# Optimization experiments

Measured on AMD Instinct MI355X. Metric: run time of the kernel, lower is better.

## Reference

```python
import jax, jax.numpy as jnp
import numpy as np
import math

C_S = 384; C_Z = 128; C_H = 16; H = 12; PQ = 4; PV = 8; C_SURF = 16
N_RES = 512; N_SURF = 2048; B = 1
INF = 1e5; EPS = 1e-8
SOFTPLUS_INV_1 = 0.541324854612918


def _quat_to_rot(q):
    q = q / jnp.linalg.norm(q, axis=-1, keepdims=True)
    w, x, y, z = q[..., 0], q[..., 1], q[..., 2], q[..., 3]
    R = jnp.stack([
        1 - 2 * (y * y + z * z), 2 * (x * y - w * z), 2 * (x * z + w * y),
        2 * (x * y + w * z), 1 - 2 * (x * x + z * z), 2 * (y * z - w * x),
        2 * (x * z - w * y), 2 * (y * z + w * x), 1 - 2 * (x * x + y * y),
    ], axis=-1)
    return R.reshape(q.shape[:-1] + (3, 3))


def setup_inputs() -> dict:
    key = jax.random.key(0)
    ks = jax.random.split(key, 32)
    hc = H * C_H            # 192
    hpq = H * PQ * 3        # 144
    hpkv = H * (PQ + PV) * 3  # 432
    cz4 = C_Z // 4
    concat = hc + H * PV * 3 + H * PV + H * cz4 + hc  # 1152
    w = lambda k, i, o: jax.random.normal(k, (i, o), jnp.float32) * 0.02
    inp = {
        's': jax.random.normal(ks[0], (B, N_RES, C_S), jnp.float32),
        'z': jax.random.normal(ks[1], (B, N_RES, N_RES, C_Z), jnp.float32),
        'rots': _quat_to_rot(jax.random.normal(ks[2], (B, N_RES, 4), jnp.float32)),
        'trans': jax.random.normal(ks[3], (B, N_RES, 3), jnp.float32) * 10.0,
        'mask': jnp.ones((B, N_RES), jnp.float32),
        'surface_points': jax.random.normal(ks[4], (B, N_SURF, 3), jnp.float32) * 10.0,
        'surface_features': jax.random.normal(ks[5], (B, N_SURF, C_SURF), jnp.float32),
        'surface_mask': jnp.ones((B, N_SURF), jnp.float32),
        'Wq': w(ks[6], C_S, hc), 'bq': jnp.zeros((hc,)),
        'Wkv': w(ks[7], C_S, 2 * hc), 'bkv': jnp.zeros((2 * hc,)),
        'Wqp': w(ks[8], C_S, hpq), 'bqp': jnp.zeros((hpq,)),
        'Wkvp': w(ks[9], C_S, hpkv), 'bkvp': jnp.zeros((hpkv,)),
        'Wse': w(ks[10], C_SURF, C_S), 'bse': jnp.zeros((C_S,)),
        'Wsq': w(ks[11], C_S, hc), 'bsq': jnp.zeros((hc,)),
        'Wsk': w(ks[12], C_S, hc), 'bsk': jnp.zeros((hc,)),
        'Wsv': w(ks[13], C_S, hc), 'bsv': jnp.zeros((hc,)),
        'Wb': w(ks[14], C_Z, H), 'bb': jnp.zeros((H,)),
        'Wdz': w(ks[15], C_Z, cz4), 'bdz': jnp.zeros((cz4,)),
        'head_weights': jnp.full((H,), SOFTPLUS_INV_1, jnp.float32),
        'sb_weights': jnp.full((1,), SOFTPLUS_INV_1, jnp.float32),
        'Wout': w(ks[16], concat, C_S), 'bout': jnp.zeros((C_S,)),
        'Wso': w(ks[17], 2 * C_S, C_SURF), 'bso': jnp.zeros((C_SURF,)),
    }
    return inp


def reference(s, z, rots, trans, mask, surface_points, surface_features, surface_mask,
              Wq, bq, Wkv, bkv, Wqp, bqp, Wkvp, bkvp, Wse, bse, Wsq, bsq, Wsk, bsk,
              Wsv, bsv, Wb, bb, Wdz, bdz, head_weights, sb_weights, Wout, bout, Wso, bso):
    lin = lambda x, W, b: x @ W + b
    b_, n, _ = s.shape
    m = surface_points.shape[-2]

    surface_feat = lin(surface_features, Wse, bse)                    # [B,M,c_s]
    # backbone<->surface squared distances
    disp = trans[:, :, None, :] - surface_points[:, None, :, :]       # [B,N,M,3]
    dist_sq = jnp.sum(disp * disp, -1)                                # [B,N,M]

    q = lin(s, Wq, bq).reshape(b_, n, H, C_H)
    kv = lin(s, Wkv, bkv).reshape(b_, n, H, 2 * C_H)
    k, v = kv[..., :C_H], kv[..., C_H:]

    # query points: split into 3 coord chunks, stack, rigid-apply
    qp = lin(s, Wqp, bqp)
    qp = jnp.stack(jnp.split(qp, 3, axis=-1), axis=-1)                # [B,N,H*PQ,3]
    qp = jnp.einsum('bnij,bnpj->bnpi', rots, qp) + trans[:, :, None]
    qp = qp.reshape(b_, n, H, PQ, 3)

    kvp = lin(s, Wkvp, bkvp)
    kvp = jnp.stack(jnp.split(kvp, 3, axis=-1), axis=-1)              # [B,N,H*(PQ+PV),3]
    kvp = jnp.einsum('bnij,bnpj->bnpi', rots, kvp) + trans[:, :, None]
    kvp = kvp.reshape(b_, n, H, PQ + PV, 3)
    kp, vp = kvp[..., :PQ, :], kvp[..., PQ:, :]

    b_bias = lin(z, Wb, bb)                                           # [B,N,N,H]
    a = jnp.einsum('bihc,bjhc->bhij', q, k) * math.sqrt(1.0 / (3 * C_H))
    a = a + math.sqrt(1.0 / 3) * jnp.transpose(b_bias, (0, 3, 1, 2))

    # point-distance attention term
    pt = jnp.sum((qp[:, :, None] - kp[:, None]) ** 2, axis=-1)        # [B,N,N,H,PQ]
    hw = jax.nn.softplus(head_weights)                                # [H]
    pt = jnp.sum(pt, axis=-1) * hw * math.sqrt(1.0 / (3 * (PQ * 9.0 / 2))) * (-0.5)
    a = a + jnp.transpose(pt, (0, 3, 1, 2))                           # [B,H,N,N]

    sq_mask = INF * (mask[:, :, None] * mask[:, None, :] - 1.0)
    a = jax.nn.softmax(a + sq_mask[:, None], axis=-1)

    o = jnp.einsum('bhij,bjhc->bihc', a, v).reshape(b_, n, H * C_H)
    o_pt = jnp.einsum('bhij,bjhpd->bihpd', a, vp)                     # [B,N,H,PV,3]
    o_pt = jnp.einsum('bnji,bnhpj->bnhpi', rots, o_pt - trans[:, :, None, None])
    o_pt_norm = jnp.sqrt(jnp.sum(o_pt ** 2, -1) + EPS).reshape(b_, n, H * PV)
    o_pt_flat = o_pt.reshape(b_, n, H * PV, 3)

    pair_z = lin(z, Wdz, bdz)                                         # [B,N,N,cz/4]
    o_pair = jnp.einsum('bhij,bijc->bihc', a, pair_z).reshape(b_, n, -1)

    # surface cross-attention branch
    sq = lin(s, Wsq, bsq).reshape(b_, n, H, C_H)
    sk = lin(surface_feat, Wsk, bsk).reshape(b_, m, H, C_H)
    sv = lin(surface_feat, Wsv, bsv).reshape(b_, m, H, C_H)
    logits = jnp.einsum('bnhc,bmhc->bhnm', sq, sk) * math.sqrt(1.0 / C_H)
    sbw = jax.nn.softplus(sb_weights)[0]
    logits = logits - 0.5 * sbw * dist_sq[:, None]
    cross_mask = mask[:, :, None] * surface_mask[:, None, :]          # [B,N,M]
    logits = logits + INF * (cross_mask - 1.0)[:, None]
    a_s = jax.nn.softmax(logits, axis=-1)
    o_surf = jnp.einsum('bhnm,bmhc->bnhc', a_s, sv).reshape(b_, n, H * C_H)

    o_cat = jnp.concatenate([o, o_pt_flat[..., 0], o_pt_flat[..., 1], o_pt_flat[..., 2],
                             o_pt_norm, o_pair, o_surf], axis=-1)
    s_out = lin(o_cat, Wout, bout)                                    # [B,N,c_s]

    # surface update: attend surface points to backbone (softmax over residues)
    a_ts = jax.nn.softmax(jnp.swapaxes(logits, -1, -2), axis=-1).mean(axis=1)  # [B,M,N]
    s_agg = jnp.einsum('bmn,bnc->bmc', a_ts, s)
    surf_out = lin(jnp.concatenate([surface_feat, s_agg], axis=-1), Wso, bso)
    return s_out, surf_out
```

## Files before the change

kernel.cpp:

```cpp
#include <hip/hip_runtime.h>
#include <cstddef>


#define CS 384
#define INFV 100000.0f

__device__ __forceinline__ float softplusf(float x) { return log1pf(__expf(x)); }

__global__ __launch_bounds__(256) void k_pack(
    const float* __restrict__ Wq, const float* __restrict__ Wsq,
    const float* __restrict__ Wkv, const float* __restrict__ Wqp,
    const float* __restrict__ Wkvp, const float* __restrict__ Wsk,
    const float* __restrict__ Wsv, const float* __restrict__ Wout,
    const float* __restrict__ bq, const float* __restrict__ bsq,
    const float* __restrict__ bkv, const float* __restrict__ bqp,
    const float* __restrict__ bkvp, const float* __restrict__ bsk,
    const float* __restrict__ bsv,
    float* __restrict__ wt1, float* __restrict__ wt2, float* __restrict__ wt3,
    float* __restrict__ b1, float* __restrict__ b2)
{
    const int b = blockIdx.x, t = threadIdx.x;
    if (b >= 1092) {
        int idx = (b - 1092) * 256 + t;
        if (idx < 1344) {
            float v;
            if (idx < 192) v = bq[idx];
            else if (idx < 384) v = bsq[idx - 192];
            else if (idx < 768) v = bkv[idx - 384];
            else if (idx < 912) v = bqp[idx - 768];
            else v = bkvp[idx - 912];
            b1[idx] = v;
        } else if (idx < 1728) {
            int i2 = idx - 1344;
            b2[i2] = (i2 < 192) ? bsk[i2] : bsv[i2 - 192];
        }
        return;
    }
    const float* src; float* dst; int C, coff, tile, ldd;
    if (b < 72)       { src = Wq;   C = 192; dst = wt1; coff = 0;   ldd = 384;  tile = b; }
    else if (b < 144) { src = Wsq;  C = 192; dst = wt1; coff = 192; ldd = 384;  tile = b - 72; }
    else if (b < 288) { src = Wkv;  C = 384; dst = wt1; coff = 384; ldd = 384;  tile = b - 144; }
    else if (b < 348) { src = Wqp;  C = 144; dst = wt1; coff = 768; ldd = 384;  tile = b - 288; }
    else if (b < 516) { src = Wkvp; C = 432; dst = wt1; coff = 912; ldd = 384;  tile = b - 348; }
    else if (b < 588) { src = Wsk;  C = 192; dst = wt2; coff = 0;   ldd = 384;  tile = b - 516; }
    else if (b < 660) { src = Wsv;  C = 192; dst = wt2; coff = 192; ldd = 384;  tile = b - 588; }
    else              { src = Wout; C = 384; dst = wt3; coff = 0;   ldd = 1152; tile = b - 660; }
    const int cT = (C + 31) >> 5;
    const int tk = tile / cT, tc = tile % cT;
    __shared__ float l[32][33];
    const int tr = t >> 5, tcc = t & 31;
    #pragma unroll
    for (int rr = 0; rr < 4; ++rr) {
        int kloc = tr * 4 + rr;
        int cg = tc * 32 + tcc;
        l[kloc][tcc] = (cg < C) ? src[(size_t)(tk * 32 + kloc) * C + cg] : 0.f;
    }
    __syncthreads();
    #pragma unroll
    for (int rr = 0; rr < 4; ++rr) {
        int cloc = tr * 4 + rr;
        int cg = tc * 32 + cloc;
        if (cg < C) dst[(size_t)(coff + cg) * ldd + tk * 32 + tcc] = l[tcc][cloc];
    }
}

__global__ __launch_bounds__(256) void k_packz(
    const float* __restrict__ Wb, const float* __restrict__ bb,
    const float* __restrict__ Wdz, const float* __restrict__ bdz,
    float* __restrict__ wz, float* __restrict__ bz)
{
    const float s3 = 0.5773502691896258f;
    int idx = blockIdx.x * 256 + threadIdx.x;
    if (idx < 5632) {
        int c = idx >> 7, kk = idx & 127;
        wz[idx] = (c < 12) ? s3 * Wb[kk * 12 + c] : Wdz[kk * 32 + (c - 12)];
    } else if (idx < 5676) {
        int c = idx - 5632;
        bz[c] = (c < 12) ? s3 * bb[c] : bdz[c - 12];
    }
}

__global__ __launch_bounds__(256) void k_transp(
    const float* __restrict__ A, float* __restrict__ At)
{
    __shared__ float tile[32][33];
    const int r0 = blockIdx.y * 32, c0 = blockIdx.x * 32;
    const int tr = threadIdx.x >> 5, tc = threadIdx.x & 31;
    #pragma unroll
    for (int rr = 0; rr < 4; ++rr)
        tile[tr + rr * 8][tc] = A[(size_t)(r0 + tr + rr * 8) * 384 + c0 + tc];
    __syncthreads();
    #pragma unroll
    for (int rr = 0; rr < 4; ++rr)
        At[(size_t)(c0 + tr + rr * 8) * 512 + r0 + tc] = tile[tc][tr + rr * 8];
}

template<int KTOT, bool HB>
__global__ __launch_bounds__(256) void k_gemm(
    const float* __restrict__ A, const float* __restrict__ Wt,
    const float* __restrict__ bias, float* __restrict__ C, int ldc)
{
    __shared__ float As[64][68];
    __shared__ float Ws[64][68];
    const int t = threadIdx.x;
    const int c0 = blockIdx.x * 64, m0 = blockIdx.y * 64;
    const int sr = t >> 4, sk4 = (t & 15) << 2;
    const int wid = t >> 6, lane = t & 63;
    const int wr = (wid >> 1) * 32, wc = (wid & 1) * 32;
    const int lr = lane >> 3, lc = lane & 7;
    float acc[4][4];
    #pragma unroll
    for (int j = 0; j < 4; ++j) {
        float bv = HB ? bias[c0 + wc + lc + 8 * j] : 0.f;
        #pragma unroll
        for (int i = 0; i < 4; ++i) acc[i][j] = bv;
    }
    for (int kc = 0; kc < KTOT; kc += 64) {
        __syncthreads();
        #pragma unroll
        for (int rep = 0; rep < 4; ++rep) {
            int row = sr + rep * 16;
            *(float4*)&As[row][sk4] = *(const float4*)&A[(size_t)(m0 + row) * KTOT + kc + sk4];
            *(float4*)&Ws[row][sk4] = *(const float4*)&Wt[(size_t)(c0 + row) * KTOT + kc + sk4];
        }
        __syncthreads();
        #pragma unroll 4
        for (int k4 = 0; k4 < 16; ++k4) {
            float4 a[4], w[4];
            #pragma unroll
            for (int i = 0; i < 4; ++i) a[i] = *(float4*)&As[wr + lr + 8 * i][k4 * 4];
            #pragma unroll
            for (int j = 0; j < 4; ++j) w[j] = *(float4*)&Ws[wc + lc + 8 * j][k4 * 4];
            #pragma unroll
            for (int i = 0; i < 4; ++i) {
                #pragma unroll
                for (int j = 0; j < 4; ++j) {
                    acc[i][j] = fmaf(a[i].x, w[j].x, acc[i][j]);
                    acc[i][j] = fmaf(a[i].y, w[j].y, acc[i][j]);
                    acc[i][j] = fmaf(a[i].z, w[j].z, acc[i][j]);
                    acc[i][j] = fmaf(a[i].w, w[j].w, acc[i][j]);
                }
            }
        }
    }
    #pragma unroll
    for (int i = 0; i < 4; ++i) {
        #pragma unroll
        for (int j = 0; j < 4; ++j)
            C[(size_t)(m0 + wr + lr + 8 * i) * ldc + c0 + wc + lc + 8 * j] = acc[i][j];
    }
}

__global__ __launch_bounds__(256) void k_scatter(
    const float* __restrict__ proj, const float* __restrict__ rots,
    const float* __restrict__ trans,
    float* __restrict__ qw, float* __restrict__ kw, float* __restrict__ vw,
    float* __restrict__ sqw, float* __restrict__ qpw, float* __restrict__ kpw,
    float* __restrict__ vpw)
{
    __shared__ float p[4][1344];
    const int n0 = blockIdx.x * 4, t = threadIdx.x;
    for (int idx = t; idx < 1344; idx += 256) {
        #pragma unroll
        for (int r = 0; r < 4; ++r) p[r][idx] = proj[(size_t)(n0 + r) * 1344 + idx];
    }
    __syncthreads();
    for (int idx = t; idx < 3072; idx += 256) {
        int r = idx / 768, c = idx % 768;
        int n = n0 + r;
        float v = p[r][c];
        if (c < 192) qw[(size_t)n * 192 + c] = v;
        else if (c < 384) sqw[(size_t)n * 192 + (c - 192)] = v;
        else {
            int cc = c - 384, h = cc >> 5, sub = cc & 31;
            if (sub < 16) kw[(size_t)n * 192 + h * 16 + sub] = v;
            else          vw[(size_t)n * 192 + h * 16 + (sub - 16)] = v;
        }
    }
    for (int idx = t; idx < 2304; idx += 256) {
        int r = idx / 576, rem = idx % 576;
        int n = n0 + r;
        const float* R = &rots[(size_t)n * 9];
        const float* tr = &trans[(size_t)n * 3];
        if (rem < 144) {
            int pp = rem / 3, d = rem % 3;
            float v = fmaf(R[d*3+0], p[r][768 + pp],
                      fmaf(R[d*3+1], p[r][768 + 48 + pp],
                      fmaf(R[d*3+2], p[r][768 + 96 + pp], tr[d])));
            qpw[(size_t)n * 144 + pp * 3 + d] = v;
        } else {
            int rem2 = rem - 144; int pp = rem2 / 3, d = rem2 % 3;
            float v = fmaf(R[d*3+0], p[r][912 + pp],
                      fmaf(R[d*3+1], p[r][912 + 144 + pp],
                      fmaf(R[d*3+2], p[r][912 + 288 + pp], tr[d])));
            int h = pp / 12, ii = pp % 12;
            if (ii < 4) kpw[(size_t)n * 144 + h * 12 + ii * 3 + d] = v;
            else        vpw[(size_t)n * 288 + h * 24 + (ii - 4) * 3 + d] = v;
        }
    }
}

__global__ __launch_bounds__(256) void k_sfeat(
    const float* __restrict__ sf, const float* __restrict__ Wse,
    const float* __restrict__ bse, float* __restrict__ sfeat)
{
    __shared__ float wl[16 * 384];
    __shared__ float sfl[8][16];
    const int m0 = blockIdx.x * 8, t = threadIdx.x;
    for (int idx = t; idx < 6144; idx += 256) wl[idx] = Wse[idx];
    if (t < 128) sfl[t >> 4][t & 15] = sf[(size_t)(m0 + (t >> 4)) * 16 + (t & 15)];
    __syncthreads();
    #pragma unroll
    for (int u = 0; u < 12; ++u) {
        int idx = t + u * 256;
        int r = idx / 384, c = idx % 384;
        float a = bse[c];
        #pragma unroll
        for (int kk = 0; kk < 16; ++kk) a = fmaf(sfl[r][kk], wl[kk * 384 + c], a);
        sfeat[(size_t)(m0 + r) * 384 + c] = a;
    }
}

__global__ __launch_bounds__(256) void k_zpass(
    const float* __restrict__ z, const float* __restrict__ wz,
    const float* __restrict__ bz, float* __restrict__ bpz)
{
    __shared__ float zt[64][132];
    const int i = blockIdx.x, t = threadIdx.x;
    const int jbase = blockIdx.y * 256;
    const int jl = t & 63;
    const int cgs = __builtin_amdgcn_readfirstlane(t >> 6);
    const float* __restrict__ wp = wz + cgs * 11 * 128;
    float bv[11];
    #pragma unroll
    for (int u = 0; u < 11; ++u) bv[u] = bz[cgs * 11 + u];
    for (int ch = 0; ch < 4; ++ch) {
        const int j0 = jbase + ch * 64;
        __syncthreads();
        for (int idx = t; idx < 2048; idx += 256) {
            int r = idx >> 5, c4 = (idx & 31) << 2;
            *(float4*)&zt[r][c4] = *(const float4*)&z[((size_t)i * 512 + j0 + r) * 128 + c4];
        }
        __syncthreads();
        float acc[11];
        #pragma unroll
        for (int u = 0; u < 11; ++u) acc[u] = bv[u];
        #pragma unroll 2
        for (int k4 = 0; k4 < 128; k4 += 4) {
            float4 zv = *(float4*)&zt[jl][k4];
            #pragma unroll
            for (int u = 0; u < 11; ++u) {
                const float* w = wp + u * 128 + k4;
                acc[u] = fmaf(zv.x, w[0],
                         fmaf(zv.y, w[1],
                         fmaf(zv.z, w[2],
                         fmaf(zv.w, w[3], acc[u]))));
            }
        }
        #pragma unroll
        for (int u = 0; u < 11; ++u)
            bpz[((size_t)i * 44 + cgs * 11 + u) * 512 + j0 + jl] = acc[u];
    }
}

__global__ __launch_bounds__(256) void k_attn_a(
    const float* __restrict__ qw, const float* __restrict__ kw,
    const float* __restrict__ qpw, const float* __restrict__ kpw,
    const float* __restrict__ bpz, const float* __restrict__ mask,
    const float* __restrict__ hwp, float* __restrict__ abuf)
{
    __shared__ float pls[4][520];
    __shared__ float qs[64], qps[48], cpt4[4];
    const int i = blockIdx.x, hg = blockIdx.y;
    const int t = threadIdx.x;
    if (t < 64) qs[t] = qw[(size_t)i * 192 + hg * 64 + t];
    if (t < 48) qps[t] = qpw[(size_t)i * 144 + hg * 48 + t];
    if (t < 4) cpt4[t] = -0.5f * 0.13608276348795434f * softplusf(hwp[hg * 4 + t]);
    const float mask_i = mask[i];
    __syncthreads();
    #pragma unroll 2
    for (int it = 0; it < 8; ++it) {
        int idx = t + it * 256;
        int hh = idx >> 9, j = idx & 511;
        int h = hg * 4 + hh;
        float kj[16], kpj[12];
        { const float4* kr = (const float4*)&kw[(size_t)j * 192 + h * 16];
          *(float4*)&kj[0] = kr[0]; *(float4*)&kj[4] = kr[1];
          *(float4*)&kj[8] = kr[2]; *(float4*)&kj[12] = kr[3]; }
        { const float4* kr = (const float4*)&kpw[(size_t)j * 144 + h * 12];
          *(float4*)&kpj[0] = kr[0]; *(float4*)&kpj[4] = kr[1]; *(float4*)&kpj[8] = kr[2]; }
        float qk = 0.f;
        #pragma unroll
        for (int c = 0; c < 16; ++c) qk = fmaf(qs[hh * 16 + c], kj[c], qk);
        float pts = 0.f;
        #pragma unroll
        for (int p = 0; p < 4; ++p) {
            float dx = qps[hh*12+p*3+0] - kpj[p*3+0];
            float dy = qps[hh*12+p*3+1] - kpj[p*3+1];
            float dz = qps[hh*12+p*3+2] - kpj[p*3+2];
            pts += dx*dx + dy*dy + dz*dz;
        }
        float lg = fmaf(0.14433756729740643f, qk, bpz[((size_t)i * 44 + h) * 512 + j]);
        lg = fmaf(cpt4[hh], pts, lg);
        lg += INFV * (mask_i * mask[j] - 1.0f);
        pls[hh][j] = lg;
    }
    __syncthreads();
    const int w = t >> 6, lane = t & 63;
    float v[8];
    #pragma unroll
    for (int k = 0; k < 8; ++k) v[k] = pls[w][lane + k * 64];
    float mx = v[0];
    #pragma unroll
    for (int k = 1; k < 8; ++k) mx = fmaxf(mx, v[k]);
    #pragma unroll
    for (int off = 32; off; off >>= 1) mx = fmaxf(mx, __shfl_xor(mx, off));
    float sm = 0.f;
    #pragma unroll
    for (int k = 0; k < 8; ++k) { v[k] = __expf(v[k] - mx); sm += v[k]; }
    #pragma unroll
    for (int off = 32; off; off >>= 1) sm += __shfl_xor(sm, off);
    const float inv = 1.0f / sm;
    float* dst = abuf + ((size_t)(hg * 4 + w) * 512 + i) * 512;
    #pragma unroll
    for (int k = 0; k < 8; ++k) dst[lane + k * 64] = v[k] * inv;
}

__global__ __launch_bounds__(256) void k_attn_pair(
    const float* __restrict__ abuf, const float* __restrict__ bpz,
    float* __restrict__ ocat)
{
    __shared__ float al[12][512];
    const int i = blockIdx.x, t = threadIdx.x;
    #pragma unroll
    for (int u = 0; u < 12; ++u) {
        al[u][t] = abuf[(size_t)u * 262144 + (size_t)i * 512 + t];
        al[u][t + 256] = abuf[(size_t)u * 262144 + (size_t)i * 512 + t + 256];
    }
    __syncthreads();
    const int c = t & 31;
    const int h1 = t >> 5;
    const bool dual = (t < 128);
    const float* pz = bpz + ((size_t)i * 44 + 12 + c) * 512;
    const float* a1 = al[h1];
    const float* a2 = al[dual ? h1 + 8 : 0];
    float acc1 = 0.f, acc2 = 0.f;
    for (int j = 0; j < 512; j += 4) {
        float4 p = *(const float4*)&pz[j];
        acc1 = fmaf(a1[j+0], p.x, acc1);
        acc1 = fmaf(a1[j+1], p.y, acc1);
        acc1 = fmaf(a1[j+2], p.z, acc1);
        acc1 = fmaf(a1[j+3], p.w, acc1);
        if (dual) {
            acc2 = fmaf(a2[j+0], p.x, acc2);
            acc2 = fmaf(a2[j+1], p.y, acc2);
            acc2 = fmaf(a2[j+2], p.z, acc2);
            acc2 = fmaf(a2[j+3], p.w, acc2);
        }
    }
    ocat[(size_t)i * 1152 + 576 + h1 * 32 + c] = acc1;
    if (dual) ocat[(size_t)i * 1152 + 576 + (h1 + 8) * 32 + c] = acc2;
}

__global__ __launch_bounds__(256) void k_gemm_ov(
    const float* __restrict__ abuf, const float* __restrict__ vw,
    const float* __restrict__ vpw, float* __restrict__ cbuf)
{
    __shared__ float As[64][68];
    __shared__ float Bs[64][44];
    const int i0 = blockIdx.x * 64, h = blockIdx.y;
    const int t = threadIdx.x;
    const int sr = t >> 4, sk4 = (t & 15) << 2;
    const int r1 = t >> 3;
    const int cb = t & 7;
    float acc[2][5];
    #pragma unroll
    for (int u = 0; u < 5; ++u) { acc[0][u] = 0.f; acc[1][u] = 0.f; }
    for (int kc = 0; kc < 512; kc += 64) {
        __syncthreads();
        #pragma unroll
        for (int rep = 0; rep < 4; ++rep) {
            int row = sr + rep * 16;
            *(float4*)&As[row][sk4] =
                *(const float4*)&abuf[(size_t)h * 262144 + (size_t)(i0 + row) * 512 + kc + sk4];
        }
        #pragma unroll
        for (int u = 0; u < 10; ++u) {
            int idx = t + u * 256;
            int r = idx / 40, cc = idx % 40;
            Bs[r][cc] = (cc < 16) ? vw[(size_t)(kc + r) * 192 + h * 16 + cc]
                                  : vpw[(size_t)(kc + r) * 288 + h * 24 + (cc - 16)];
        }
        __syncthreads();
        #pragma unroll 4
        for (int kk = 0; kk < 64; ++kk) {
            float av1 = As[r1][kk], av2 = As[r1 + 32][kk];
            #pragma unroll
            for (int u = 0; u < 5; ++u) {
                float b = Bs[kk][cb + 8 * u];
                acc[0][u] = fmaf(av1, b, acc[0][u]);
                acc[1][u] = fmaf(av2, b, acc[1][u]);
            }
        }
    }
    #pragma unroll
    for (int u = 0; u < 5; ++u) {
        cbuf[((size_t)h * 512 + i0 + r1) * 40 + cb + 8 * u] = acc[0][u];
        cbuf[((size_t)h * 512 + i0 + r1 + 32) * 40 + cb + 8 * u] = acc[1][u];
    }
}

__global__ __launch_bounds__(256) void k_optfin(
    const float* __restrict__ cbuf, const float* __restrict__ rots,
    const float* __restrict__ trans, float* __restrict__ ocat)
{
    __shared__ float cl[4][12][40];
    const int i0 = blockIdx.x * 4, t = threadIdx.x;
    for (int idx = t; idx < 1920; idx += 256) {
        int ii = idx / 480, rem = idx % 480;
        int h = rem / 40, c = rem % 40;
        cl[ii][h][c] = cbuf[((size_t)h * 512 + i0 + ii) * 40 + c];
    }
    __syncthreads();
    for (int idx = t; idx < 768; idx += 256) {
        int ii = idx / 192, o = idx % 192;
        ocat[(size_t)(i0 + ii) * 1152 + o] = cl[ii][o >> 4][o & 15];
    }
    for (int idx = t; idx < 384; idx += 256) {
        int ii = idx / 96, hp = idx % 96;
        int h = hp >> 3, p = hp & 7;
        int i = i0 + ii;
        const float* R = &rots[(size_t)i * 9];
        float gx = cl[ii][h][16 + p*3 + 0] - trans[(size_t)i*3 + 0];
        float gy = cl[ii][h][16 + p*3 + 1] - trans[(size_t)i*3 + 1];
        float gz = cl[ii][h][16 + p*3 + 2] - trans[(size_t)i*3 + 2];
        float lx = R[0]*gx + R[3]*gy + R[6]*gz;
        float ly = R[1]*gx + R[4]*gy + R[7]*gz;
        float lz = R[2]*gx + R[5]*gy + R[8]*gz;
        float nm = sqrtf(lx*lx + ly*ly + lz*lz + 1e-8f);
        int col = h * 8 + p;
        size_t base = (size_t)i * 1152;
        ocat[base + 192 + col] = lx;
        ocat[base + 288 + col] = ly;
        ocat[base + 384 + col] = lz;
        ocat[base + 480 + col] = nm;
    }
}

__global__ __launch_bounds__(256) void k_tlog(
    const float* __restrict__ sqw, const float* __restrict__ skv,
    const float* __restrict__ trans, const float* __restrict__ mask,
    const float* __restrict__ sp, const float* __restrict__ smask,
    const float* __restrict__ sbwp, float* __restrict__ logits,
    float* __restrict__ stat_m, float* __restrict__ stat_il)
{
    __shared__ float sk_s[32][16];
    __shared__ float sq_s[32][16];
    __shared__ float trans_s[96];
    __shared__ float mask_s[32];
    __shared__ float spm_s[96];
    __shared__ float smask_s[32];
    const int h = blockIdx.y;
    const int m0 = blockIdx.x * 32;
    const int t = threadIdx.x;
    const int tmg = t >> 5, tnl = t & 31;
    const float sbw = softplusf(sbwp[0]);
    for (int idx = t; idx < 512; idx += 256) {
        int row = idx >> 4, c = idx & 15;
        sk_s[row][c] = skv[(size_t)(m0 + row) * 384 + h * 16 + c];
    }
    if (t < 96) spm_s[t] = sp[(size_t)m0 * 3 + t];
    if (t < 32) smask_s[t] = smask[m0 + t];
    __syncthreads();
    float skr[4][16];
    float spx[4], spy[4], spz[4], smk[4];
    #pragma unroll
    for (int mi = 0; mi < 4; ++mi) {
        int row = tmg * 4 + mi;
        #pragma unroll
        for (int c4 = 0; c4 < 16; c4 += 4)
            *(float4*)&skr[mi][c4] = *(float4*)&sk_s[row][c4];
        spx[mi] = spm_s[row*3+0]; spy[mi] = spm_s[row*3+1]; spz[mi] = spm_s[row*3+2];
        smk[mi] = smask_s[row];
    }
    float mxr[4], lr[4];
    #pragma unroll
    for (int mi = 0; mi < 4; ++mi) { mxr[mi] = -1e30f; lr[mi] = 0.f; }
    for (int nt = 0; nt < 16; ++nt) {
        __syncthreads();
        const int nb = nt * 32;
        if (t < 128) {
            int nn = t >> 2, c4 = (t & 3) << 2;
            *(float4*)&sq_s[nn][c4] = *(const float4*)&sqw[(size_t)(nb + nn) * 192 + h * 16 + c4];
        }
        if (t < 96) trans_s[t] = trans[(size_t)nb * 3 + t];
        if (t < 32) mask_s[t] = mask[nb + t];
        __syncthreads();
        float q[16];
        #pragma unroll
        for (int c4 = 0; c4 < 16; c4 += 4)
            *(float4*)&q[c4] = *(float4*)&sq_s[tnl][c4];
        const float tx = trans_s[tnl*3+0], ty = trans_s[tnl*3+1], tz = trans_s[tnl*3+2];
        const float mkn = mask_s[tnl];
        #pragma unroll
        for (int mi = 0; mi < 4; ++mi) {
            float dot = 0.f;
            #pragma unroll
            for (int c = 0; c < 16; ++c) dot = fmaf(skr[mi][c], q[c], dot);
            float dx = tx - spx[mi], dy = ty - spy[mi], dz = tz - spz[mi];
            float mterm = INFV * (mkn * smk[mi] - 1.0f) - 0.5f * sbw * (dx*dx + dy*dy + dz*dz);
            float lg = fmaf(0.25f, dot, mterm);
            logits[((size_t)(m0 + tmg * 4 + mi) * 12 + h) * 512 + nb + tnl] = lg;
            float newm = fmaxf(mxr[mi], lg);
            lr[mi] = lr[mi] * __expf(mxr[mi] - newm) + __expf(lg - newm);
            mxr[mi] = newm;
        }
    }
    #pragma unroll
    for (int off = 1; off < 32; off <<= 1) {
        #pragma unroll
        for (int mi = 0; mi < 4; ++mi) {
            float m2 = __shfl_xor(mxr[mi], off), l2 = __shfl_xor(lr[mi], off);
            float newm = fmaxf(mxr[mi], m2);
            lr[mi] = lr[mi] * __expf(mxr[mi] - newm) + l2 * __expf(m2 - newm);
            mxr[mi] = newm;
        }
    }
    if (tnl == 0) {
        #pragma unroll
        for (int mi = 0; mi < 4; ++mi) {
            int m = m0 + tmg * 4 + mi;
            stat_m[(size_t)m * 12 + h] = mxr[mi];
            stat_il[(size_t)m * 12 + h] = 1.0f / lr[mi];
        }
    }
}

__global__ __launch_bounds__(256) void k_rstat(
    const float* __restrict__ lbuf, float* __restrict__ rspm,
    float* __restrict__ rsps)
{
    __shared__ float smx[4][64], ssm[4][64];
    const int n0 = blockIdx.x * 64, mc = blockIdx.y, h = blockIdx.z;
    const int t = threadIdx.x, ln = t & 63, mg = t >> 6;
    const int mb = mc * 512;
    const int n = n0 + ln;
    float mx = -1e30f, sm = 0.f;
    #pragma unroll 2
    for (int it = 0; it < 128; ++it) {
        int m = mb + it * 4 + mg;
        float lg = lbuf[((size_t)m * 12 + h) * 512 + n];
        float nm = fmaxf(mx, lg);
        sm = sm * __expf(mx - nm) + __expf(lg - nm);
        mx = nm;
    }
    smx[mg][ln] = mx; ssm[mg][ln] = sm;
    __syncthreads();
    if (t < 64) {
        float M = smx[0][t], S = ssm[0][t];
        #pragma unroll
        for (int g = 1; g < 4; ++g) {
            float m2 = smx[g][t], s2 = ssm[g][t];
            float nm = fmaxf(M, m2);
            S = S * __expf(M - nm) + s2 * __expf(m2 - nm);
            M = nm;
        }
        rspm[((size_t)h * 4 + mc) * 512 + n0 + t] = M;
        rsps[((size_t)h * 4 + mc) * 512 + n0 + t] = S;
    }
}

__global__ __launch_bounds__(256) void k_rcomb(
    const float* __restrict__ rspm, const float* __restrict__ rsps,
    float* __restrict__ rmax, float* __restrict__ rinv)
{
    int gid = blockIdx.x * 256 + threadIdx.x;
    if (gid >= 6144) return;
    int h = gid >> 9, n = gid & 511;
    float M = -1e30f, S = 0.f;
    #pragma unroll
    for (int mc = 0; mc < 4; ++mc) {
        float m2 = rspm[((size_t)h * 4 + mc) * 512 + n];
        float s2 = rsps[((size_t)h * 4 + mc) * 512 + n];
        float nm = fmaxf(M, m2);
        S = S * __expf(M - nm) + s2 * __expf(m2 - nm);
        M = nm;
    }
    rmax[gid] = M;
    rinv[gid] = 1.0f / S;
}

__global__ __launch_bounds__(256) void k_pv(
    const float* __restrict__ lbuf, const float* __restrict__ skv,
    const float* __restrict__ rmax, const float* __restrict__ rinv,
    float* __restrict__ pvp)
{
    __shared__ float sv_s[512][17];
    const int n0 = blockIdx.x * 64, mc = blockIdx.y, h = blockIdx.z;
    const int t = threadIdx.x, ln = t & 63, mg = t >> 6;
    const int mb = mc * 512;
    for (int idx = t; idx < 2048; idx += 256) {
        int ml = idx >> 2, c4 = (idx & 3) << 2;
        float4 v4 = *(const float4*)&skv[(size_t)(mb + ml) * 384 + 192 + h * 16 + c4];
        sv_s[ml][c4+0]=v4.x; sv_s[ml][c4+1]=v4.y; sv_s[ml][c4+2]=v4.z; sv_s[ml][c4+3]=v4.w;
    }
    const int n = n0 + ln;
    const float rm = rmax[h * 512 + n], ri = rinv[h * 512 + n];
    float acc[16];
    #pragma unroll
    for (int c = 0; c < 16; ++c) acc[c] = 0.f;
    __syncthreads();
    #pragma unroll 2
    for (int it = 0; it < 128; ++it) {
        int ml = it * 4 + mg;
        float w = __expf(lbuf[((size_t)(mb + ml) * 12 + h) * 512 + n] - rm) * ri;
        #pragma unroll
        for (int c = 0; c < 16; ++c) acc[c] = fmaf(w, sv_s[ml][c], acc[c]);
    }
    __syncthreads();
    float* red = &sv_s[0][0];
    #pragma unroll
    for (int c = 0; c < 16; ++c) red[(mg * 64 + ln) * 17 + c] = acc[c];
    __syncthreads();
    {
        int nl = t >> 2, c4 = (t & 3) << 2;
        float4 o;
        #pragma unroll
        for (int e = 0; e < 4; ++e) {
            float s = 0.f;
            #pragma unroll
            for (int g = 0; g < 4; ++g) s += red[(g * 64 + nl) * 17 + c4 + e];
            (&o.x)[e] = s;
        }
        *(float4*)&pvp[(((size_t)h * 4 + mc) * 512 + n0 + nl) * 16 + c4] = o;
    }
}

__global__ __launch_bounds__(256) void k_pvcomb(
    const float* __restrict__ pvp, float* __restrict__ ocat)
{
    int gid = blockIdx.x * 256 + threadIdx.x;
    int n = gid / 192, rem = gid % 192;
    float o = 0.f;
    #pragma unroll
    for (int mc = 0; mc < 4; ++mc)
        o += pvp[(((size_t)(rem >> 4) * 4 + mc) * 512 + n) * 16 + (rem & 15)];
    ocat[(size_t)n * 1152 + 960 + rem] = o;
}

__global__ __launch_bounds__(256) void k_tw(
    const float* __restrict__ logits, const float* __restrict__ stat_m,
    const float* __restrict__ stat_il, float* __restrict__ w)
{
    __shared__ float mxs[12], ils[12];
    const int m = blockIdx.x, t = threadIdx.x;
    if (t < 12) { mxs[t] = stat_m[(size_t)m * 12 + t]; ils[t] = stat_il[(size_t)m * 12 + t]; }
    __syncthreads();
    const float* lp = logits + (size_t)m * 12 * 512;
    float a0 = 0.f, a1 = 0.f;
    #pragma unroll
    for (int h = 0; h < 12; ++h) {
        a0 += __expf(lp[h * 512 + t] - mxs[h]) * ils[h];
        a1 += __expf(lp[h * 512 + 256 + t] - mxs[h]) * ils[h];
    }
    w[(size_t)m * 512 + t] = a0 * (1.0f / 12.0f);
    w[(size_t)m * 512 + 256 + t] = a1 * (1.0f / 12.0f);
}

__global__ __launch_bounds__(256) void k_surf_out(
    const float* __restrict__ sfeat, const float* __restrict__ saggw,
    const float* __restrict__ Wso, const float* __restrict__ bso,
    float* __restrict__ out)
{
    __shared__ float wl[12304];
    const int t = threadIdx.x;
    for (int idx = t; idx < 12288; idx += 256) {
        int k = idx >> 4, c = idx & 15;
        wl[(k / 192) * 3076 + (k % 192) * 16 + c] = Wso[idx];
    }
    const int m = blockIdx.x * 64 + (t >> 2);
    const int kq = t & 3;
    const float* src = (kq < 2) ? &sfeat[(size_t)m * 384 + kq * 192]
                                : &saggw[(size_t)m * 384 + (kq - 2) * 192];
    __syncthreads();
    float acc[16];
    #pragma unroll
    for (int c = 0; c < 16; ++c) acc[c] = 0.f;
    const float* wb = &wl[kq * 3076];
    for (int k = 0; k < 192; k += 4) {
        float4 v = *(const float4*)&src[k];
        #pragma unroll
        for (int e = 0; e < 4; ++e) {
            float sv = (&v.x)[e];
            #pragma unroll
            for (int c = 0; c < 16; ++c)
                acc[c] = fmaf(sv, wb[(k + e) * 16 + c], acc[c]);
        }
    }
    #pragma unroll
    for (int c = 0; c < 16; ++c) {
        acc[c] += __shfl_xor(acc[c], 1);
        acc[c] += __shfl_xor(acc[c], 2);
    }
    #pragma unroll
    for (int c = 0; c < 16; ++c) {
        if ((c >> 2) == kq) out[196608 + (size_t)m * 16 + c] = acc[c] + bso[c];
    }
}

extern "C" void kernel_launch(void* const* d_in, const int* in_sizes, int n_in,
                              void* d_out, int out_size, void* d_ws, size_t ws_size,
                              hipStream_t stream)
{
    (void)in_sizes; (void)n_in; (void)out_size; (void)ws_size;
    const float* s     = (const float*)d_in[0];
    const float* z     = (const float*)d_in[1];
    const float* rots  = (const float*)d_in[2];
    const float* trans = (const float*)d_in[3];
    const float* mask  = (const float*)d_in[4];
    const float* sp    = (const float*)d_in[5];
    const float* sf    = (const float*)d_in[6];
    const float* smask = (const float*)d_in[7];
    const float* Wq    = (const float*)d_in[8];  const float* bq   = (const float*)d_in[9];
    const float* Wkv   = (const float*)d_in[10]; const float* bkv  = (const float*)d_in[11];
    const float* Wqp   = (const float*)d_in[12]; const float* bqp  = (const float*)d_in[13];
    const float* Wkvp  = (const float*)d_in[14]; const float* bkvp = (const float*)d_in[15];
    const float* Wse   = (const float*)d_in[16]; const float* bse  = (const float*)d_in[17];
    const float* Wsq   = (const float*)d_in[18]; const float* bsq  = (const float*)d_in[19];
    const float* Wsk   = (const float*)d_in[20]; const float* bsk  = (const float*)d_in[21];
    const float* Wsv   = (const float*)d_in[22]; const float* bsv  = (const float*)d_in[23];
    const float* Wb    = (const float*)d_in[24]; const float* bb   = (const float*)d_in[25];
    const float* Wdz   = (const float*)d_in[26]; const float* bdz  = (const float*)d_in[27];
    const float* hw    = (const float*)d_in[28]; const float* sbw  = (const float*)d_in[29];
    const float* Wout  = (const float*)d_in[30]; const float* bout = (const float*)d_in[31];
    const float* Wso   = (const float*)d_in[32]; const float* bso  = (const float*)d_in[33];
    float* out = (float*)d_out;

    float* qw    = (float*)d_ws;
    float* kw    = qw    + (size_t)512 * 192;
    float* vw    = kw    + (size_t)512 * 192;
    float* sqw   = vw    + (size_t)512 * 192;
    float* qpw   = sqw   + (size_t)512 * 192;
    float* kpw   = qpw   + (size_t)512 * 144;
    float* vpw   = kpw   + (size_t)512 * 144;
    float* sfeat = vpw   + (size_t)512 * 288;
    float* skv   = sfeat + (size_t)2048 * 384;
    float* ocat  = skv   + (size_t)2048 * 384;
    float* sagg  = ocat  + (size_t)512 * 1152;
    float* region = sagg + (size_t)2048 * 384;
    float* proj   = region;
    float* bpz    = region;
    float* logits = region;
    float* wt1   = region + (size_t)2048 * 12 * 512;
    float* wt2   = wt1   + (size_t)1344 * 384;
    float* wt3   = wt2   + (size_t)384 * 384;
    float* b1    = wt3   + (size_t)384 * 1152;
    float* b2    = b1    + 1344;
    float* st    = b2    + 384;
    float* wbuf  = st    + (size_t)384 * 512;
    float* statm = wbuf  + (size_t)2048 * 512;
    float* stati = statm + (size_t)2048 * 12;
    float* abuf  = stati + (size_t)2048 * 12;
    float* cbuf  = abuf  + (size_t)12 * 512 * 512;
    float* wz    = cbuf  + (size_t)12 * 512 * 40;
    float* bz    = wz    + (size_t)44 * 128;
    float* rspm  = bz    + 64;
    float* rsps  = rspm  + (size_t)12 * 4 * 512;
    float* rmax  = rsps  + (size_t)12 * 4 * 512;
    float* rinv  = rmax  + (size_t)12 * 512;
    float* pvp   = rinv  + (size_t)12 * 512;

    k_pack<<<dim3(1099), dim3(256), 0, stream>>>(Wq, Wsq, Wkv, Wqp, Wkvp, Wsk, Wsv, Wout,
        bq, bsq, bkv, bqp, bkvp, bsk, bsv, wt1, wt2, wt3, b1, b2);
    k_packz<<<dim3(23), dim3(256), 0, stream>>>(Wb, bb, Wdz, bdz, wz, bz);
    k_transp<<<dim3(12, 16), dim3(256), 0, stream>>>(s, st);
    k_gemm<384, true><<<dim3(21, 8), dim3(256), 0, stream>>>(s, wt1, b1, proj, 1344);
    k_scatter<<<dim3(128), dim3(256), 0, stream>>>(proj, rots, trans,
        qw, kw, vw, sqw, qpw, kpw, vpw);
    k_sfeat<<<dim3(256), dim3(256), 0, stream>>>(sf, Wse, bse, sfeat);
    k_gemm<384, true><<<dim3(6, 32), dim3(256), 0, stream>>>(sfeat, wt2, b2, skv, 384);
    k_zpass<<<dim3(512, 2), dim3(256), 0, stream>>>(z, wz, bz, bpz);
    k_attn_a<<<dim3(512, 3), dim3(256), 0, stream>>>(qw, kw, qpw, kpw, bpz, mask, hw, abuf);
    k_attn_pair<<<dim3(512), dim3(256), 0, stream>>>(abuf, bpz, ocat);
    k_gemm_ov<<<dim3(8, 12), dim3(256), 0, stream>>>(abuf, vw, vpw, cbuf);
    k_optfin<<<dim3(128), dim3(256), 0, stream>>>(cbuf, rots, trans, ocat);
    k_tlog<<<dim3(64, 12), dim3(256), 0, stream>>>(sqw, skv, trans, mask, sp, smask,
        sbw, logits, statm, stati);
    k_rstat<<<dim3(8, 4, 12), dim3(256), 0, stream>>>(logits, rspm, rsps);
    k_rcomb<<<dim3(24), dim3(256), 0, stream>>>(rspm, rsps, rmax, rinv);
    k_pv<<<dim3(8, 4, 12), dim3(256), 0, stream>>>(logits, skv, rmax, rinv, pvp);
    k_pvcomb<<<dim3(384), dim3(256), 0, stream>>>(pvp, ocat);
    k_tw<<<dim3(2048), dim3(256), 0, stream>>>(logits, statm, stati, wbuf);
    k_gemm<512, false><<<dim3(6, 32), dim3(256), 0, stream>>>(wbuf, st, nullptr, sagg, 384);
    k_surf_out<<<dim3(32), dim3(256), 0, stream>>>(sfeat, sagg, Wso, bso, out);
    k_gemm<1152, true><<<dim3(6, 8), dim3(256), 0, stream>>>(ocat, wt3, bout, out, 384);
}
```

Baseline: 524.1 us.

## Stage z-projection weights in LDS and split zpass into one 64-row tile per block

```diff
diff --git a/kernel.cpp b/kernel.cpp
--- a/kernel.cpp
+++ b/kernel.cpp
@@ -226,41 +226,50 @@
     const float* __restrict__ bz, float* __restrict__ bpz)
 {
     __shared__ float zt[64][132];
-    const int i = blockIdx.x, t = threadIdx.x;
-    const int jbase = blockIdx.y * 256;
+    __shared__ float wt[44 * 128];
+    const int t = threadIdx.x;
+    const int jg0 = blockIdx.x * 64;
+    const int i = jg0 >> 9;
+    const int jloc = jg0 & 511;
     const int jl = t & 63;
     const int cgs = __builtin_amdgcn_readfirstlane(t >> 6);
-    const float* __restrict__ wp = wz + cgs * 11 * 128;
+    #pragma unroll
+    for (int u = 0; u < 6; ++u) {
+        int idx = t + u * 256;
+        if (idx < 1408) *(float4*)&wt[idx * 4] = *(const float4*)&wz[idx * 4];
+    }
+    #pragma unroll
+    for (int u = 0; u < 8; ++u) {
+        int idx = t + u * 256;
+        int r = idx >> 5, c4 = (idx & 31) << 2;
+        *(float4*)&zt[r][c4] = *(const float4*)&z[((size_t)(jg0 + r)) * 128 + c4];
+    }
     float bv[11];
     #pragma unroll
     for (int u = 0; u < 11; ++u) bv[u] = bz[cgs * 11 + u];
-    for (int ch = 0; ch < 4; ++ch) {
-        const int j0 = jbase + ch * 64;
-        __syncthreads();
-        for (int idx = t; idx < 2048; idx += 256) {
-            int r = idx >> 5, c4 = (idx & 31) << 2;
-            *(float4*)&zt[r][c4] = *(const float4*)&z[((size_t)i * 512 + j0 + r) * 128 + c4];
-        }
-        __syncthreads();
-        float acc[11];
-        #pragma unroll
-        for (int u = 0; u < 11; ++u) acc[u] = bv[u];
-        #pragma unroll 2
-        for (int k4 = 0; k4 < 128; k4 += 4) {
-            float4 zv = *(float4*)&zt[jl][k4];
-            #pragma unroll
-            for (int u = 0; u < 11; ++u) {
-                const float* w = wp + u * 128 + k4;
-                acc[u] = fmaf(zv.x, w[0],
-                         fmaf(zv.y, w[1],
-                         fmaf(zv.z, w[2],
-                         fmaf(zv.w, w[3], acc[u]))));
-            }
-        }
+    __syncthreads();
+    float acc[11];
+    #pragma unroll
+    for (int u = 0; u < 11; ++u) acc[u] = bv[u];
+    const float* wbase = &wt[cgs * 11 * 128];
+    #pragma unroll 4
+    for (int k4 = 0; k4 < 128; k4 += 4) {
+        float4 zv = *(float4*)&zt[jl][k4];
+        float4 wv[11];
         #pragma unroll
         for (int u = 0; u < 11; ++u)
-            bpz[((size_t)i * 44 + cgs * 11 + u) * 512 + j0 + jl] = acc[u];
-    }
+            wv[u] = *(const float4*)&wbase[u * 128 + k4];
+        #pragma unroll
+        for (int u = 0; u < 11; ++u) {
+            acc[u] = fmaf(zv.x, wv[u].x, acc[u]);
+            acc[u] = fmaf(zv.y, wv[u].y, acc[u]);
+            acc[u] = fmaf(zv.z, wv[u].z, acc[u]);
+            acc[u] = fmaf(zv.w, wv[u].w, acc[u]);
+        }
+    }
+    #pragma unroll
+    for (int u = 0; u < 11; ++u)
+        bpz[((size_t)i * 44 + cgs * 11 + u) * 512 + jloc + jl] = acc[u];
 }
 
 __global__ __launch_bounds__(256) void k_attn_a(
@@ -779,7 +788,7 @@
         qw, kw, vw, sqw, qpw, kpw, vpw);
     k_sfeat<<<dim3(256), dim3(256), 0, stream>>>(sf, Wse, bse, sfeat);
     k_gemm<384, true><<<dim3(6, 32), dim3(256), 0, stream>>>(sfeat, wt2, b2, skv, 384);
-    k_zpass<<<dim3(512, 2), dim3(256), 0, stream>>>(z, wz, bz, bpz);
+    k_zpass<<<dim3(4096), dim3(256), 0, stream>>>(z, wz, bz, bpz);
     k_attn_a<<<dim3(512, 3), dim3(256), 0, stream>>>(qw, kw, qpw, kpw, bpz, mask, hw, abuf);
     k_attn_pair<<<dim3(512), dim3(256), 0, stream>>>(abuf, bpz, ocat);
     k_gemm_ov<<<dim3(8, 12), dim3(256), 0, stream>>>(abuf, vw, vpw, cbuf);
```

After: 549.4 us. +4.8%, slower.
